# Optimization experiments

Hardware: AMD Instinct MI355X
Metric: run time of the kernel (lower is better)

Reference implementation:

```python
import jax, jax.numpy as jnp
import numpy as np

B, S, EMBED, DK, DV, M = 8, 1024, 1024, 512, 512, 64


def setup_inputs() -> dict:
    key = jax.random.key(0)
    ks = jax.random.split(key, 9)
    query_in = jax.random.normal(ks[0], (B, S, EMBED), dtype=jnp.float32)
    key_in = jax.random.normal(ks[1], (B, S, EMBED), dtype=jnp.float32)
    value_in = jax.random.normal(ks[2], (B, S, EMBED), dtype=jnp.float32)
    lim = 1.0 / np.sqrt(EMBED)  # nn.Linear default init range
    u = lambda k, shape: jax.random.uniform(k, shape, minval=-lim, maxval=lim, dtype=jnp.float32)
    return {
        'query_in': query_in, 'key_in': key_in, 'value_in': value_in,
        'Wq': u(ks[3], (DK, EMBED)), 'bq': u(ks[4], (DK,)),
        'Wk': u(ks[5], (DK, EMBED)), 'bk': u(ks[6], (DK,)),
        'Wv': u(ks[7], (DV, EMBED)), 'bv': u(ks[8], (DV,)),
    }


def _select_landmarks(k_proj, m):
    # Original code runs recursive RLS sampling (random, host-side) over the m
    # segment-rows of key.reshape(B, m, seg, d) and gathers m of them back,
    # then flattens to (B, S, d). We use a deterministic data-dependent
    # selection (rows ranked by squared norm) with identical gather structure.
    Bb, Ss, d = k_proj.shape
    seg = Ss // m
    kr = k_proj.reshape(Bb, m, seg, d)
    scores = jnp.sum(kr * kr, axis=(2, 3))                      # [B, m]
    idx = jnp.argsort(-scores, axis=1)                          # [B, m]
    land = jnp.take_along_axis(kr, idx[:, :, None, None], axis=1)
    return land.reshape(Bb, Ss, d)                              # [B, S, d]


def reference(query_in, key_in, value_in, Wq, bq, Wk, bk, Wv, bv):
    scaling = DK ** -0.25  # 1/sqrt(sqrt(d_k)), applied to both q and k
    q = (jnp.einsum('bse,de->bsd', query_in, Wq) + bq) * scaling
    k = (jnp.einsum('bse,de->bsd', key_in, Wk) + bk) * scaling
    v = jnp.einsum('bse,de->bsd', value_in, Wv) + bv

    kl = _select_landmarks(k, M)                                # [B, S, DK]
    # is_decoder_self_attn is hard-coded True upstream -> q_landmarks = q,
    # so kernel_2 == kernel_1.
    kernel_1 = jax.nn.softmax(jnp.einsum('bqd,bkd->bqk', q, kl), axis=-1)
    kernel_2 = kernel_1
    kernel_3 = jax.nn.softmax(jnp.einsum('bqd,bkd->bqk', q, k), axis=-1)

    k2_inv = jnp.linalg.pinv(kernel_2)                          # [B, S, S] batched SVD
    out = jnp.einsum('bqk,bkd->bqd', jnp.einsum('bqm,bmk->bqk', kernel_1, k2_inv),
                     jnp.einsum('bqk,bkd->bqd', kernel_3, v))
    # dropout is identity in eval mode
    return out
```

## Files before the change

### kernel.cpp

```cpp
#include <hip/hip_runtime.h>
#include <hip/hip_bf16.h>

#define SS   1024
#define DKK  512

typedef __hip_bfloat16 bf16;
typedef __attribute__((ext_vector_type(8))) short s16x8;
typedef __attribute__((ext_vector_type(8))) unsigned short u16x8;
typedef __attribute__((ext_vector_type(4))) float f32x4;

#define WS_ST    (40ull << 20)
#define WS_W(z)  ((48ull << 20) + ((size_t)(z) << 20))
#define WS_Q     (52ull << 20)
#define WS_K     (60ull << 20)
#define WS_VT    (68ull << 20)
#define WS_LG    (0ull)

__device__ __forceinline__ void async_ld16(const void* g, void* s) {
  __builtin_amdgcn_global_load_lds(
      (const __attribute__((address_space(1))) void*)g,
      (__attribute__((address_space(3))) void*)s, 16, 0, 0);
}

__device__ __forceinline__ unsigned short f2bfu(float f) {
  return __builtin_bit_cast(unsigned short, __float2bfloat16(f));
}
__device__ __forceinline__ float bfu2f(unsigned short u) {
  unsigned int i = ((unsigned int)u) << 16;
  return __builtin_bit_cast(float, i);
}

__global__ __launch_bounds__(256)
void convert_w(const float* __restrict__ w0, const float* __restrict__ w1,
               const float* __restrict__ w2, char* __restrict__ ws)
{
  const int bx = blockIdx.x;
  const int z = bx >> 8, local = bx & 255;
  const float* src = (z == 0) ? w0 : (z == 1) ? w1 : w2;
  unsigned short* dst = (unsigned short*)(ws + WS_W(z));
  const int i = local * 2048 + threadIdx.x * 8;
  const float4* s = (const float4*)(src + i);
  float4 a = s[0], b = s[1];
  ushort4 o0, o1;
  o0.x = f2bfu(a.x); o0.y = f2bfu(a.y); o0.z = f2bfu(a.z); o0.w = f2bfu(a.w);
  o1.x = f2bfu(b.x); o1.y = f2bfu(b.y); o1.z = f2bfu(b.z); o1.w = f2bfu(b.w);
  ((ushort4*)(dst + i))[0] = o0;
  ((ushort4*)(dst + i))[1] = o1;
}

template<int BM, int BN, int K, int LDA, int LDB>
__device__ __forceinline__ void gemm_core(const bf16* __restrict__ A,
                                          const bf16* __restrict__ Bw,
                                          int bm, int bn,
                                          short* As, short* Bs, f32x4* acc)
{
  constexpr int MI = BM / 32, NI = BN / 32;
  constexpr int AR = BM / 4,  BR = BN / 4;
  const int tid  = threadIdx.x;
  const int lane = tid & 63;
  const int wave = tid >> 6;
  const int l8   = lane >> 3;
  const int kch  = ((lane & 7) ^ l8) * 8;
  const bf16* ag = A  + (size_t)(bm * BM + wave * AR + l8) * LDA + kch;
  const bf16* bg = Bw + (size_t)(bn * BN + wave * BR + l8) * LDB + kch;
  short* AsW = As + wave * AR * 64;
  short* BsW = Bs + wave * BR * 64;
  const int waveM = wave >> 1, waveN = wave & 1;
  const int l16  = lane & 15;
  const int quad = lane >> 4;
  const int xr   = l16 & 7;

  #pragma unroll
  for (int t = 0; t < MI * NI; ++t)
    #pragma unroll
    for (int r = 0; r < 4; ++r) acc[t][r] = 0.0f;

  for (int kt = 0; kt < K / 64; ++kt) {
    #pragma unroll
    for (int j = 0; j < AR / 8; ++j) async_ld16(ag + (size_t)j * 8 * LDA, AsW + j * 8 * 64);
    #pragma unroll
    for (int j = 0; j < BR / 8; ++j) async_ld16(bg + (size_t)j * 8 * LDB, BsW + j * 8 * 64);
    ag += 64; bg += 64;
    __syncthreads();
    #pragma unroll
    for (int ks = 0; ks < 2; ++ks) {
      s16x8 af[MI], bfv[NI];
      #pragma unroll
      for (int mi = 0; mi < MI; ++mi) {
        const int row  = waveM * (BM / 2) + mi * 16 + l16;
        const int slot = (ks * 4 + quad) ^ xr;
        af[mi] = *(const s16x8*)&As[row * 64 + slot * 8];
      }
      #pragma unroll
      for (int ni = 0; ni < NI; ++ni) {
        const int row  = waveN * (BN / 2) + ni * 16 + l16;
        const int slot = (ks * 4 + quad) ^ xr;
        bfv[ni] = *(const s16x8*)&Bs[row * 64 + slot * 8];
      }
      #pragma unroll
      for (int mi = 0; mi < MI; ++mi)
        #pragma unroll
        for (int ni = 0; ni < NI; ++ni)
          acc[mi * NI + ni] = __builtin_amdgcn_mfma_f32_16x16x32_bf16(
              af[mi], bfv[ni], acc[mi * NI + ni], 0, 0, 0);
    }
    __syncthreads();
  }
}

template<int K, int LDA, int LDB>
__device__ __forceinline__ void gemm_core_f32a(const float* __restrict__ A,
                                               const bf16* __restrict__ Bw,
                                               int bm, int bn,
                                               short* As, short* Bs, f32x4* acc)
{
  const int tid  = threadIdx.x;
  const int lane = tid & 63;
  const int wave = tid >> 6;
  const int l8   = lane >> 3;
  const int kch  = ((lane & 7) ^ l8) * 8;
  const bf16* bg = Bw + (size_t)(bn * 256 + wave * 64 + l8) * LDB + kch;
  short* BsW = Bs + wave * 64 * 64;
  const int arow = tid >> 3;
  const int ag8  = tid & 7;
  const int slotA = (ag8 ^ (arow & 7)) * 8;
  const float* agp = A + (size_t)(bm * 64 + arow) * LDA + ag8 * 8;
  const int waveM = wave >> 1, waveN = wave & 1;
  const int l16  = lane & 15;
  const int quad = lane >> 4;
  const int xr   = l16 & 7;

  #pragma unroll
  for (int t = 0; t < 16; ++t)
    #pragma unroll
    for (int r = 0; r < 4; ++r) acc[t][r] = 0.0f;

  float4 a0 = ((const float4*)agp)[0], b0 = ((const float4*)agp)[1];
  float4 a1 = ((const float4*)(agp + 32 * LDA))[0];
  float4 b1 = ((const float4*)(agp + 32 * LDA))[1];
  agp += 64;

  for (int kt = 0; kt < K / 64; ++kt) {
    #pragma unroll
    for (int j = 0; j < 8; ++j) async_ld16(bg + (size_t)j * 8 * LDB, BsW + j * 8 * 64);
    bg += 64;
    u16x8 v0, v1;
    v0[0] = f2bfu(a0.x); v0[1] = f2bfu(a0.y); v0[2] = f2bfu(a0.z); v0[3] = f2bfu(a0.w);
    v0[4] = f2bfu(b0.x); v0[5] = f2bfu(b0.y); v0[6] = f2bfu(b0.z); v0[7] = f2bfu(b0.w);
    v1[0] = f2bfu(a1.x); v1[1] = f2bfu(a1.y); v1[2] = f2bfu(a1.z); v1[3] = f2bfu(a1.w);
    v1[4] = f2bfu(b1.x); v1[5] = f2bfu(b1.y); v1[6] = f2bfu(b1.z); v1[7] = f2bfu(b1.w);
    *(u16x8*)&As[arow * 64 + slotA] = v0;
    *(u16x8*)&As[(32 + arow) * 64 + slotA] = v1;
    if (kt != K / 64 - 1) {
      a0 = ((const float4*)agp)[0]; b0 = ((const float4*)agp)[1];
      a1 = ((const float4*)(agp + 32 * LDA))[0];
      b1 = ((const float4*)(agp + 32 * LDA))[1];
    }
    agp += 64;
    __syncthreads();
    #pragma unroll
    for (int ks = 0; ks < 2; ++ks) {
      s16x8 af[2], bfv[8];
      #pragma unroll
      for (int mi = 0; mi < 2; ++mi) {
        const int row  = waveM * 32 + mi * 16 + l16;
        const int slot = (ks * 4 + quad) ^ xr;
        af[mi] = *(const s16x8*)&As[row * 64 + slot * 8];
      }
      #pragma unroll
      for (int ni = 0; ni < 8; ++ni) {
        const int row  = waveN * 128 + ni * 16 + l16;
        const int slot = (ks * 4 + quad) ^ xr;
        bfv[ni] = *(const s16x8*)&Bs[row * 64 + slot * 8];
      }
      #pragma unroll
      for (int mi = 0; mi < 2; ++mi)
        #pragma unroll
        for (int ni = 0; ni < 8; ++ni)
          acc[mi * 8 + ni] = __builtin_amdgcn_mfma_f32_16x16x32_bf16(
              af[mi], bfv[ni], acc[mi * 8 + ni], 0, 0, 0);
    }
    __syncthreads();
  }
}

__global__ __launch_bounds__(256, 3)
void proj_kernel(const float* __restrict__ Xq, const float* __restrict__ Xk,
                 const float* __restrict__ Xv, const bf16* __restrict__ W0,
                 const float* __restrict__ bq, const float* __restrict__ bk,
                 const float* __restrict__ bv,
                 bf16* __restrict__ qo, bf16* __restrict__ ko,
                 bf16* __restrict__ vT, float qscale)
{
  __shared__ __align__(16) short As[64 * 64];
  __shared__ __align__(16) short Bs[256 * 64];
  const int id   = blockIdx.x;
  const int xcd  = id & 7;
  const int s    = id >> 3;
  const int bn   = s & 1;
  const int pair = (s >> 1) * 8 + xcd;
  const int bm   = pair & 127;
  const int z    = pair >> 7;
  const float* A  = (z == 0) ? Xq : (z == 1) ? Xk : Xv;
  const bf16*  Bw = W0 + ((size_t)z << 19);
  const float* bias = (z == 0) ? bq : (z == 1) ? bk : bv;
  f32x4 acc[16];
  gemm_core_f32a<1024, 1024, 1024>(A, Bw, bm, bn, As, Bs, acc);

  const int lane = threadIdx.x & 63;
  const int wave = threadIdx.x >> 6;
  const int waveM = wave >> 1, waveN = wave & 1;
  const int l16 = lane & 15, quad = lane >> 4;
  const int row0 = bm * 64 + waveM * 32;
  const int col0 = bn * 256 + waveN * 128;
  const float sc = (z == 0) ? qscale : 1.0f;
  bf16* C = (z == 0) ? qo : ko;
  #pragma unroll
  for (int ni = 0; ni < 8; ++ni) {
    const int col = col0 + ni * 16 + l16;
    const float bb = bias[col];
    #pragma unroll
    for (int mi = 0; mi < 2; ++mi)
      #pragma unroll
      for (int r = 0; r < 4; ++r) {
        const int row = row0 + mi * 16 + quad * 4 + r;
        const float v = acc[mi * 8 + ni][r] + bb;
        if (z == 2)
          vT[((size_t)(row >> 10) * DKK + col) * SS + (row & (SS - 1))] =
              __float2bfloat16(v);
        else
          C[(size_t)row * DKK + col] = __float2bfloat16(v * sc);
      }
  }
}

__global__ __launch_bounds__(256, 8)
void scores_kernel(const bf16* __restrict__ q, const bf16* __restrict__ k,
                   unsigned short* __restrict__ Pp, float* __restrict__ stats)
{
  __shared__ __align__(16) short As[64 * 64];
  __shared__ __align__(16) short Bs[64 * 64];
  const int z = blockIdx.z;
  const int bn = blockIdx.x, bm = blockIdx.y;
  f32x4 acc[4];
  gemm_core<64, 64, 512, 512, 512>(q + (size_t)z * SS * DKK,
                                   k + (size_t)z * SS * DKK,
                                   bm, bn, As, Bs, acc);

  const int lane = threadIdx.x & 63;
  const int wave = threadIdx.x >> 6;
  const int waveM = wave >> 1, waveN = wave & 1;
  const int l16 = lane & 15, quad = lane >> 4;
  const int row0 = bm * 64 + waveM * 32;
  const int col0 = bn * 64 + waveN * 32;
  const int chunk = bn * 2 + waveN;
  unsigned short* C = Pp + (size_t)z * SS * SS;
  #pragma unroll
  for (int mi = 0; mi < 2; ++mi)
    #pragma unroll
    for (int r = 0; r < 4; ++r) {
      const int row = row0 + mi * 16 + quad * 4 + r;
      const float x0 = acc[mi * 2 + 0][r], x1 = acc[mi * 2 + 1][r];
      float m = fmaxf(x0, x1);
      #pragma unroll
      for (int msk = 1; msk < 16; msk <<= 1) m = fmaxf(m, __shfl_xor(m, msk));
      const float e0 = __expf(x0 - m), e1 = __expf(x1 - m);
      float ssum = e0 + e1;
      #pragma unroll
      for (int msk = 1; msk < 16; msk <<= 1) ssum += __shfl_xor(ssum, msk);
      C[(size_t)row * SS + col0 + l16]      = f2bfu(e0);
      C[(size_t)row * SS + col0 + 16 + l16] = f2bfu(e1);
      if (l16 == 0) {
        float2 mr; mr.x = m; mr.y = ssum;
        *(float2*)&stats[(((size_t)z * SS + row) * 32 + chunk) * 2] = mr;
      }
    }
}

__device__ __forceinline__ void gemm_core_pvs(const unsigned short* __restrict__ Pp,
                                              const bf16* __restrict__ vT,
                                              int bm, int bn, const float* Fl,
                                              short* As, short* Bs, f32x4* acc)
{
  const int tid  = threadIdx.x;
  const int lane = tid & 63;
  const int wave = tid >> 6;
  const int l8   = lane >> 3;
  const int kch  = ((lane & 7) ^ l8) * 8;
  const bf16* bg = vT + (size_t)(bn * 64 + wave * 16 + l8) * 1024 + kch;
  short* BsW = Bs + wave * 16 * 64;
  const int arow = tid >> 3;
  const int ag8  = tid & 7;
  const int slotA = (ag8 ^ (arow & 7)) * 8;
  const unsigned short* ag = Pp + (size_t)(bm * 64 + arow) * 1024 + ag8 * 8;
  const int waveM = wave >> 1, waveN = wave & 1;
  const int l16  = lane & 15;
  const int quad = lane >> 4;
  const int xr   = l16 & 7;

  #pragma unroll
  for (int t = 0; t < 4; ++t)
    #pragma unroll
    for (int r = 0; r < 4; ++r) acc[t][r] = 0.0f;

  u16x8 u0 = *(const u16x8*)ag;
  u16x8 u1 = *(const u16x8*)(ag + 32 * 1024);
  ag += 64;

  for (int kt = 0; kt < 16; ++kt) {
    #pragma unroll
    for (int j = 0; j < 2; ++j) async_ld16(bg + (size_t)j * 8 * 1024, BsW + j * 8 * 64);
    bg += 64;
    const int ch = kt * 2 + (ag8 >> 2);
    const float f0 = Fl[arow * 33 + ch];
    const float f1 = Fl[(32 + arow) * 33 + ch];
    u16x8 v0, v1;
    #pragma unroll
    for (int j = 0; j < 8; ++j) {
      v0[j] = f2bfu(bfu2f((unsigned short)u0[j]) * f0);
      v1[j] = f2bfu(bfu2f((unsigned short)u1[j]) * f1);
    }
    *(u16x8*)&As[arow * 64 + slotA] = v0;
    *(u16x8*)&As[(32 + arow) * 64 + slotA] = v1;
    if (kt != 15) {
      u0 = *(const u16x8*)ag;
      u1 = *(const u16x8*)(ag + 32 * 1024);
    }
    ag += 64;
    __syncthreads();
    #pragma unroll
    for (int ks = 0; ks < 2; ++ks) {
      s16x8 af[2], bfv[2];
      #pragma unroll
      for (int mi = 0; mi < 2; ++mi) {
        const int row  = waveM * 32 + mi * 16 + l16;
        const int slot = (ks * 4 + quad) ^ xr;
        af[mi] = *(const s16x8*)&As[row * 64 + slot * 8];
      }
      #pragma unroll
      for (int ni = 0; ni < 2; ++ni) {
        const int row  = waveN * 32 + ni * 16 + l16;
        const int slot = (ks * 4 + quad) ^ xr;
        bfv[ni] = *(const s16x8*)&Bs[row * 64 + slot * 8];
      }
      #pragma unroll
      for (int mi = 0; mi < 2; ++mi)
        #pragma unroll
        for (int ni = 0; ni < 2; ++ni)
          acc[mi * 2 + ni] = __builtin_amdgcn_mfma_f32_16x16x32_bf16(
              af[mi], bfv[ni], acc[mi * 2 + ni], 0, 0, 0);
    }
    __syncthreads();
  }
}

__global__ __launch_bounds__(256, 6)
void pv_kernel(const unsigned short* __restrict__ Pp, const bf16* __restrict__ vT,
               const float* __restrict__ stats, float* __restrict__ out)
{
  __shared__ __align__(16) short As[64 * 64];
  __shared__ __align__(16) short Bs[64 * 64];
  __shared__ float Ml[64], Rl[64], Fl[64 * 33];
  const int z = blockIdx.z;
  const int bn = blockIdx.x, bm = blockIdx.y;
  const int tid = threadIdx.x;

  if (tid < 64) {
    const float* st = stats + ((size_t)z * SS + bm * 64 + tid) * 64;
    float mc[32], lc[32];
    float M = -1e30f;
    #pragma unroll
    for (int c = 0; c < 32; ++c) {
      mc[c] = st[c * 2]; lc[c] = st[c * 2 + 1];
      M = fmaxf(M, mc[c]);
    }
    float L = 0.f;
    #pragma unroll
    for (int c = 0; c < 32; ++c) L += __expf(mc[c] - M) * lc[c];
    Ml[tid] = M; Rl[tid] = 1.0f / L;
  }
  __syncthreads();
  {
    const int row = tid >> 2, c0 = (tid & 3) * 8;
    const float* st = stats + (((size_t)z * SS + bm * 64 + row) * 32 + c0) * 2;
    const float M = Ml[row], R = Rl[row];
    #pragma unroll
    for (int j = 0; j < 8; ++j)
      Fl[row * 33 + c0 + j] = __expf(st[j * 2] - M) * R;
  }
  __syncthreads();

  f32x4 acc[4];
  gemm_core_pvs(Pp + (size_t)z * SS * SS, vT + (size_t)z * DKK * SS,
                bm, bn, Fl, As, Bs, acc);

  const int lane = tid & 63;
  const int wave = tid >> 6;
  const int waveM = wave >> 1, waveN = wave & 1;
  const int l16 = lane & 15, quad = lane >> 4;
  const int row0 = bm * 64 + waveM * 32;
  const int col0 = bn * 64 + waveN * 32;
  float* C = out + (size_t)z * SS * DKK;
  #pragma unroll
  for (int ni = 0; ni < 2; ++ni) {
    const int col = col0 + ni * 16 + l16;
    #pragma unroll
    for (int mi = 0; mi < 2; ++mi)
      #pragma unroll
      for (int r = 0; r < 4; ++r) {
        const int row = row0 + mi * 16 + quad * 4 + r;
        C[(size_t)row * DKK + col] = acc[mi * 2 + ni][r];
      }
  }
}

extern "C" void kernel_launch(void* const* d_in, const int* in_sizes, int n_in,
                              void* d_out, int out_size, void* d_ws, size_t ws_size,
                              hipStream_t stream)
{
  char* ws = (char*)d_ws;
  bf16*  W0   = (bf16*)(ws + WS_W(0));
  float* stat = (float*)(ws + WS_ST);
  bf16*  q    = (bf16*)(ws + WS_Q);
  bf16*  kk   = (bf16*)(ws + WS_K);
  bf16*  vT   = (bf16*)(ws + WS_VT);
  unsigned short* Pp = (unsigned short*)(ws + WS_LG);

  const float qscale = 0.044194173824159216f;

  dim3 blk(256, 1, 1);
  hipLaunchKernelGGL(convert_w, dim3(768), blk, 0, stream,
                     (const float*)d_in[3], (const float*)d_in[5],
                     (const float*)d_in[7], ws);
  hipLaunchKernelGGL(proj_kernel, dim3(768, 1, 1), blk, 0, stream,
                     (const float*)d_in[0], (const float*)d_in[1],
                     (const float*)d_in[2], W0,
                     (const float*)d_in[4], (const float*)d_in[6],
                     (const float*)d_in[8], q, kk, vT, qscale);
  hipLaunchKernelGGL(scores_kernel, dim3(16, 16, 8), blk, 0, stream,
                     q, kk, Pp, stat);
  hipLaunchKernelGGL(pv_kernel, dim3(8, 16, 8), blk, 0, stream,
                     Pp, vT, stat, (float*)d_out);
}
```

Measured before the change: 230.4 us.

## Enlarge scores and PV tiles to 128 rows and drop register prefetch

The scores kernel moves from 64x64 to 128x128 output tiles, which halves the per-row softmax chunks to 16. The PV kernel moves to 128-row tiles, and the chunk-rescale factors are now computed in a single pass. The register double-buffer prefetch of A tiles is removed in the projection and PV GEMM cores, and A is loaded directly each iteration. The larger tiles cut redundant global loads and the stats traffic, at the cost of fewer blocks, lower occupancy and exposed load latency.

```diff
diff --git a/kernel.cpp b/kernel.cpp
--- a/kernel.cpp
+++ b/kernel.cpp
@@ -9,8 +9,8 @@
 typedef __attribute__((ext_vector_type(8))) unsigned short u16x8;
 typedef __attribute__((ext_vector_type(4))) float f32x4;
 
-#define WS_ST    (40ull << 20)
 #define WS_W(z)  ((48ull << 20) + ((size_t)(z) << 20))
+#define WS_ST    (51ull << 20)
 #define WS_Q     (52ull << 20)
 #define WS_K     (60ull << 20)
 #define WS_VT    (68ull << 20)
@@ -124,7 +124,7 @@
   const int arow = tid >> 3;
   const int ag8  = tid & 7;
   const int slotA = (ag8 ^ (arow & 7)) * 8;
-  const float* agp = A + (size_t)(bm * 64 + arow) * LDA + ag8 * 8;
+  const float* ag = A + (size_t)(bm * 64 + arow) * LDA + ag8 * 8;
   const int waveM = wave >> 1, waveN = wave & 1;
   const int l16  = lane & 15;
   const int quad = lane >> 4;
@@ -135,28 +135,20 @@
     #pragma unroll
     for (int r = 0; r < 4; ++r) acc[t][r] = 0.0f;
 
-  float4 a0 = ((const float4*)agp)[0], b0 = ((const float4*)agp)[1];
-  float4 a1 = ((const float4*)(agp + 32 * LDA))[0];
-  float4 b1 = ((const float4*)(agp + 32 * LDA))[1];
-  agp += 64;
-
   for (int kt = 0; kt < K / 64; ++kt) {
     #pragma unroll
     for (int j = 0; j < 8; ++j) async_ld16(bg + (size_t)j * 8 * LDB, BsW + j * 8 * 64);
     bg += 64;
-    u16x8 v0, v1;
-    v0[0] = f2bfu(a0.x); v0[1] = f2bfu(a0.y); v0[2] = f2bfu(a0.z); v0[3] = f2bfu(a0.w);
-    v0[4] = f2bfu(b0.x); v0[5] = f2bfu(b0.y); v0[6] = f2bfu(b0.z); v0[7] = f2bfu(b0.w);
-    v1[0] = f2bfu(a1.x); v1[1] = f2bfu(a1.y); v1[2] = f2bfu(a1.z); v1[3] = f2bfu(a1.w);
-    v1[4] = f2bfu(b1.x); v1[5] = f2bfu(b1.y); v1[6] = f2bfu(b1.z); v1[7] = f2bfu(b1.w);
-    *(u16x8*)&As[arow * 64 + slotA] = v0;
-    *(u16x8*)&As[(32 + arow) * 64 + slotA] = v1;
-    if (kt != K / 64 - 1) {
-      a0 = ((const float4*)agp)[0]; b0 = ((const float4*)agp)[1];
-      a1 = ((const float4*)(agp + 32 * LDA))[0];
-      b1 = ((const float4*)(agp + 32 * LDA))[1];
-    }
-    agp += 64;
+    #pragma unroll
+    for (int p = 0; p < 2; ++p) {
+      const float4* s = (const float4*)(ag + (size_t)p * 32 * LDA);
+      float4 a = s[0], b = s[1];
+      u16x8 v;
+      v[0] = f2bfu(a.x); v[1] = f2bfu(a.y); v[2] = f2bfu(a.z); v[3] = f2bfu(a.w);
+      v[4] = f2bfu(b.x); v[5] = f2bfu(b.y); v[6] = f2bfu(b.z); v[7] = f2bfu(b.w);
+      *(u16x8*)&As[(p * 32 + arow) * 64 + slotA] = v;
+    }
+    ag += 64;
     __syncthreads();
     #pragma unroll
     for (int ks = 0; ks < 2; ++ks) {
@@ -234,50 +226,54 @@
   }
 }
 
-__global__ __launch_bounds__(256, 8)
+__global__ __launch_bounds__(256, 3)
 void scores_kernel(const bf16* __restrict__ q, const bf16* __restrict__ k,
                    unsigned short* __restrict__ Pp, float* __restrict__ stats)
 {
-  __shared__ __align__(16) short As[64 * 64];
-  __shared__ __align__(16) short Bs[64 * 64];
+  __shared__ __align__(16) short As[128 * 64];
+  __shared__ __align__(16) short Bs[128 * 64];
   const int z = blockIdx.z;
   const int bn = blockIdx.x, bm = blockIdx.y;
-  f32x4 acc[4];
-  gemm_core<64, 64, 512, 512, 512>(q + (size_t)z * SS * DKK,
-                                   k + (size_t)z * SS * DKK,
-                                   bm, bn, As, Bs, acc);
+  f32x4 acc[16];
+  gemm_core<128, 128, 512, 512, 512>(q + (size_t)z * SS * DKK,
+                                     k + (size_t)z * SS * DKK,
+                                     bm, bn, As, Bs, acc);
 
   const int lane = threadIdx.x & 63;
   const int wave = threadIdx.x >> 6;
   const int waveM = wave >> 1, waveN = wave & 1;
   const int l16 = lane & 15, quad = lane >> 4;
-  const int row0 = bm * 64 + waveM * 32;
-  const int col0 = bn * 64 + waveN * 32;
+  const int row0 = bm * 128 + waveM * 64;
+  const int col0 = bn * 128 + waveN * 64;
   const int chunk = bn * 2 + waveN;
   unsigned short* C = Pp + (size_t)z * SS * SS;
   #pragma unroll
-  for (int mi = 0; mi < 2; ++mi)
+  for (int mi = 0; mi < 4; ++mi)
     #pragma unroll
     for (int r = 0; r < 4; ++r) {
       const int row = row0 + mi * 16 + quad * 4 + r;
-      const float x0 = acc[mi * 2 + 0][r], x1 = acc[mi * 2 + 1][r];
-      float m = fmaxf(x0, x1);
+      float x[4];
+      #pragma unroll
+      for (int ni = 0; ni < 4; ++ni) x[ni] = acc[mi * 4 + ni][r];
+      float m = fmaxf(fmaxf(x[0], x[1]), fmaxf(x[2], x[3]));
       #pragma unroll
       for (int msk = 1; msk < 16; msk <<= 1) m = fmaxf(m, __shfl_xor(m, msk));
-      const float e0 = __expf(x0 - m), e1 = __expf(x1 - m);
-      float ssum = e0 + e1;
+      float e[4], ssum = 0.f;
+      #pragma unroll
+      for (int ni = 0; ni < 4; ++ni) { e[ni] = __expf(x[ni] - m); ssum += e[ni]; }
       #pragma unroll
       for (int msk = 1; msk < 16; msk <<= 1) ssum += __shfl_xor(ssum, msk);
-      C[(size_t)row * SS + col0 + l16]      = f2bfu(e0);
-      C[(size_t)row * SS + col0 + 16 + l16] = f2bfu(e1);
+      #pragma unroll
+      for (int ni = 0; ni < 4; ++ni)
+        C[(size_t)row * SS + col0 + ni * 16 + l16] = f2bfu(e[ni]);
       if (l16 == 0) {
         float2 mr; mr.x = m; mr.y = ssum;
-        *(float2*)&stats[(((size_t)z * SS + row) * 32 + chunk) * 2] = mr;
-      }
-    }
-}
-
-__device__ __forceinline__ void gemm_core_pvs(const unsigned short* __restrict__ Pp,
+        *(float2*)&stats[(((size_t)z * SS + row) * 16 + chunk) * 2] = mr;
+      }
+    }
+}
+
+__device__ __forceinline__ void gemm_core_pvF(const unsigned short* __restrict__ Pp,
                                               const bf16* __restrict__ vT,
                                               int bm, int bn, const float* Fl,
                                               short* As, short* Bs, f32x4* acc)
@@ -292,48 +288,40 @@
   const int arow = tid >> 3;
   const int ag8  = tid & 7;
   const int slotA = (ag8 ^ (arow & 7)) * 8;
-  const unsigned short* ag = Pp + (size_t)(bm * 64 + arow) * 1024 + ag8 * 8;
+  const unsigned short* ag = Pp + (size_t)(bm * 128 + arow) * 1024 + ag8 * 8;
   const int waveM = wave >> 1, waveN = wave & 1;
   const int l16  = lane & 15;
   const int quad = lane >> 4;
   const int xr   = l16 & 7;
 
   #pragma unroll
-  for (int t = 0; t < 4; ++t)
+  for (int t = 0; t < 8; ++t)
     #pragma unroll
     for (int r = 0; r < 4; ++r) acc[t][r] = 0.0f;
-
-  u16x8 u0 = *(const u16x8*)ag;
-  u16x8 u1 = *(const u16x8*)(ag + 32 * 1024);
-  ag += 64;
 
   for (int kt = 0; kt < 16; ++kt) {
     #pragma unroll
     for (int j = 0; j < 2; ++j) async_ld16(bg + (size_t)j * 8 * 1024, BsW + j * 8 * 64);
     bg += 64;
-    const int ch = kt * 2 + (ag8 >> 2);
-    const float f0 = Fl[arow * 33 + ch];
-    const float f1 = Fl[(32 + arow) * 33 + ch];
-    u16x8 v0, v1;
-    #pragma unroll
-    for (int j = 0; j < 8; ++j) {
-      v0[j] = f2bfu(bfu2f((unsigned short)u0[j]) * f0);
-      v1[j] = f2bfu(bfu2f((unsigned short)u1[j]) * f1);
-    }
-    *(u16x8*)&As[arow * 64 + slotA] = v0;
-    *(u16x8*)&As[(32 + arow) * 64 + slotA] = v1;
-    if (kt != 15) {
-      u0 = *(const u16x8*)ag;
-      u1 = *(const u16x8*)(ag + 32 * 1024);
+    #pragma unroll
+    for (int p = 0; p < 4; ++p) {
+      const int rl = p * 32 + arow;
+      u16x8 u = *(const u16x8*)(ag + (size_t)p * 32 * 1024);
+      const float f = Fl[rl * 17 + kt];
+      u16x8 v;
+      #pragma unroll
+      for (int j = 0; j < 8; ++j)
+        v[j] = f2bfu(bfu2f((unsigned short)u[j]) * f);
+      *(u16x8*)&As[rl * 64 + slotA] = v;
     }
     ag += 64;
     __syncthreads();
     #pragma unroll
     for (int ks = 0; ks < 2; ++ks) {
-      s16x8 af[2], bfv[2];
-      #pragma unroll
-      for (int mi = 0; mi < 2; ++mi) {
-        const int row  = waveM * 32 + mi * 16 + l16;
+      s16x8 af[4], bfv[2];
+      #pragma unroll
+      for (int mi = 0; mi < 4; ++mi) {
+        const int row  = waveM * 64 + mi * 16 + l16;
         const int slot = (ks * 4 + quad) ^ xr;
         af[mi] = *(const s16x8*)&As[row * 64 + slot * 8];
       }
@@ -344,7 +332,7 @@
         bfv[ni] = *(const s16x8*)&Bs[row * 64 + slot * 8];
       }
       #pragma unroll
-      for (int mi = 0; mi < 2; ++mi)
+      for (int mi = 0; mi < 4; ++mi)
         #pragma unroll
         for (int ni = 0; ni < 2; ++ni)
           acc[mi * 2 + ni] = __builtin_amdgcn_mfma_f32_16x16x32_bf16(
@@ -354,58 +342,54 @@
   }
 }
 
-__global__ __launch_bounds__(256, 6)
+__global__ __launch_bounds__(256, 3)
 void pv_kernel(const unsigned short* __restrict__ Pp, const bf16* __restrict__ vT,
                const float* __restrict__ stats, float* __restrict__ out)
 {
-  __shared__ __align__(16) short As[64 * 64];
+  __shared__ __align__(16) short As[128 * 64];
   __shared__ __align__(16) short Bs[64 * 64];
-  __shared__ float Ml[64], Rl[64], Fl[64 * 33];
+  __shared__ float Fl[128 * 17];
   const int z = blockIdx.z;
   const int bn = blockIdx.x, bm = blockIdx.y;
   const int tid = threadIdx.x;
 
-  if (tid < 64) {
-    const float* st = stats + ((size_t)z * SS + bm * 64 + tid) * 64;
-    float mc[32], lc[32];
+  if (tid < 128) {
+    const float* st = stats + ((size_t)z * SS + bm * 128 + tid) * 32;
+    float mc[16], lc[16];
     float M = -1e30f;
     #pragma unroll
-    for (int c = 0; c < 32; ++c) {
+    for (int c = 0; c < 16; ++c) {
       mc[c] = st[c * 2]; lc[c] = st[c * 2 + 1];
       M = fmaxf(M, mc[c]);
     }
     float L = 0.f;
     #pragma unroll
-    for (int c = 0; c < 32; ++c) L += __expf(mc[c] - M) * lc[c];
-    Ml[tid] = M; Rl[tid] = 1.0f / L;
+    for (int c = 0; c < 16; ++c) {
+      mc[c] = __expf(mc[c] - M);
+      L += mc[c] * lc[c];
+    }
+    const float R = 1.0f / L;
+    #pragma unroll
+    for (int c = 0; c < 16; ++c) Fl[tid * 17 + c] = mc[c] * R;
   }
   __syncthreads();
-  {
-    const int row = tid >> 2, c0 = (tid & 3) * 8;
-    const float* st = stats + (((size_t)z * SS + bm * 64 + row) * 32 + c0) * 2;
-    const float M = Ml[row], R = Rl[row];
-    #pragma unroll
-    for (int j = 0; j < 8; ++j)
-      Fl[row * 33 + c0 + j] = __expf(st[j * 2] - M) * R;
-  }
-  __syncthreads();
-
-  f32x4 acc[4];
-  gemm_core_pvs(Pp + (size_t)z * SS * SS, vT + (size_t)z * DKK * SS,
+
+  f32x4 acc[8];
+  gemm_core_pvF(Pp + (size_t)z * SS * SS, vT + (size_t)z * DKK * SS,
                 bm, bn, Fl, As, Bs, acc);
 
   const int lane = tid & 63;
   const int wave = tid >> 6;
   const int waveM = wave >> 1, waveN = wave & 1;
   const int l16 = lane & 15, quad = lane >> 4;
-  const int row0 = bm * 64 + waveM * 32;
+  const int row0 = bm * 128 + waveM * 64;
   const int col0 = bn * 64 + waveN * 32;
   float* C = out + (size_t)z * SS * DKK;
   #pragma unroll
   for (int ni = 0; ni < 2; ++ni) {
     const int col = col0 + ni * 16 + l16;
     #pragma unroll
-    for (int mi = 0; mi < 2; ++mi)
+    for (int mi = 0; mi < 4; ++mi)
       #pragma unroll
       for (int r = 0; r < 4; ++r) {
         const int row = row0 + mi * 16 + quad * 4 + r;
@@ -437,8 +421,8 @@
                      (const float*)d_in[2], W0,
                      (const float*)d_in[4], (const float*)d_in[6],
                      (const float*)d_in[8], q, kk, vT, qscale);
-  hipLaunchKernelGGL(scores_kernel, dim3(16, 16, 8), blk, 0, stream,
+  hipLaunchKernelGGL(scores_kernel, dim3(8, 8, 8), blk, 0, stream,
                      q, kk, Pp, stat);
-  hipLaunchKernelGGL(pv_kernel, dim3(8, 16, 8), blk, 0, stream,
+  hipLaunchKernelGGL(pv_kernel, dim3(8, 8, 8), blk, 0, stream,
                      Pp, vT, stat, (float*)d_out);
 }
```

Measured after the change: 221.8 us. -3.8%, faster.
